# Optimization experiments

Measured on AMD Instinct MI355X. Metric: run time of the kernel, lower is better.

Reference implementation:

```python
import jax, jax.numpy as jnp
import numpy as np

B, S, D, H, E, K = 8, 8192, 256, 1024, 8, 2


def setup_inputs() -> dict:
    key = jax.random.key(0)
    ks = jax.random.split(key, 7)
    s_in = 1.0 / np.sqrt(D)
    s_hid = 1.0 / np.sqrt(H)
    return {
        "x": jax.random.normal(ks[0], (B, S, D), dtype=jnp.float32),
        "Wg": jax.random.uniform(ks[1], (E, D), jnp.float32, -s_in, s_in),
        "bg": jax.random.uniform(ks[2], (E,), jnp.float32, -s_in, s_in),
        "W1": jax.random.uniform(ks[3], (E, H, D), jnp.float32, -s_in, s_in),
        "b1": jax.random.uniform(ks[4], (E, H), jnp.float32, -s_in, s_in),
        "W2": jax.random.uniform(ks[5], (E, D, H), jnp.float32, -s_hid, s_hid),
        "b2": jax.random.uniform(ks[6], (E, D), jnp.float32, -s_hid, s_hid),
    }


def reference(x, Wg, bg, W1, b1, W2, b2):
    # gate: [B,S,E]
    gate_scores = jnp.einsum("bsd,ed->bse", x, Wg) + bg
    topk_scores, topk_idx = jax.lax.top_k(gate_scores, K)  # [B,S,K]
    topk_probs = jax.nn.softmax(topk_scores, axis=-1)      # [B,S,K]
    # combine weight per expert: sum over top-k slots of prob * one_hot(idx)
    combine = jnp.sum(topk_probs[..., None] * jax.nn.one_hot(topk_idx, E, dtype=x.dtype), axis=-2)  # [B,S,E]
    out = jnp.zeros_like(x)
    for e in range(E):  # small fixed loop over experts
        h = jax.nn.relu(jnp.einsum("bsd,hd->bsh", x, W1[e]) + b1[e])
        y = jnp.einsum("bsh,dh->bsd", h, W2[e]) + b2[e]
        out = out + combine[..., e:e + 1] * y
    return out
```

## Files before the change

### kernel.cpp

```cpp
#include <hip/hip_runtime.h>
#include <hip/hip_bf16.h>

#define T_TOKENS 65536
#define D_DIM 256
#define H_DIM 1024
#define E_NUM 8
#define MT 256
#define NTILE (T_TOKENS / MT)
#define HC 32
#define NCHUNK 32
#define GTB 64

typedef __attribute__((ext_vector_type(4))) float f32x4;
typedef __attribute__((ext_vector_type(8))) short s16x8;
typedef __attribute__((ext_vector_type(4))) unsigned int u32x4;
typedef __attribute__((ext_vector_type(4))) unsigned short u16x4;
typedef __attribute__((address_space(3))) unsigned int lds_u32;
typedef const __attribute__((address_space(1))) unsigned int glb_u32;

#define MFMA __builtin_amdgcn_mfma_f32_16x16x32_bf16

__device__ __forceinline__ unsigned short f2bf(float f){
  union { float f; unsigned u; } v; v.f = f;
  unsigned r = v.u + 0x7FFFu + ((v.u >> 16) & 1u);
  return (unsigned short)(r >> 16);
}
__device__ __forceinline__ float bf2f(unsigned short h){
  return __uint_as_float((unsigned)h << 16);
}
__device__ __forceinline__ unsigned cvtpk(float lo, float hi){
  unsigned r;
  asm("v_cvt_pk_bf16_f32 %0, %1, %2" : "=v"(r) : "v"(lo), "v"(hi));
  return r;
}
__device__ __forceinline__ unsigned long long pack4(f32x4 v){
  return (unsigned long long)f2bf(v.x)
       | ((unsigned long long)f2bf(v.y) << 16)
       | ((unsigned long long)f2bf(v.z) << 32)
       | ((unsigned long long)f2bf(v.w) << 48);
}

__device__ __forceinline__ void cvt_unit(int i, const float* __restrict__ W1,
                                         const float* __restrict__ W2,
                                         char* __restrict__ wsw){
  const int N1 = (E_NUM * H_DIM * D_DIM) / 4;
  unsigned long long pk;
  size_t off;
  if (i < N1){
    pk = pack4(((const f32x4*)W1)[i]);
    int idx = i << 2;
    int e  = idx >> 18;
    int h  = (idx >> 8) & (H_DIM - 1);
    int d0 = idx & (D_DIM - 1);
    int c = h >> 5, mi = (h >> 4) & 1, mrow = h & 15;
    int ks = d0 >> 5, qj = (d0 >> 3) & 3, e2 = d0 & 7;
    off = ((size_t)(e * NCHUNK + c) << 15)
        + (size_t)(((ks*2 + mi) << 10) + ((qj*16 + mrow) << 4) + (e2 << 1));
  } else {
    pk = pack4(((const f32x4*)W2)[i - N1]);
    int idx = (i - N1) << 2;
    int e   = idx >> 18;
    int d   = (idx >> 10) & (D_DIM - 1);
    int h0  = idx & (H_DIM - 1);
    int c   = h0 >> 5;
    int h32 = h0 & 31;
    int mi = (h32 >> 4) & 1, qj = (h32 >> 2) & 3;
    off = ((size_t)(e * NCHUNK + c) << 15) + 16384
        + (size_t)(((d >> 4) << 10) + ((qj * 16 + (d & 15)) << 4) + (mi << 3));
  }
  *(unsigned long long*)(wsw + off) = pk;
}

__global__ __launch_bounds__(256) void gate_kernel(
    const float* __restrict__ x, const float* __restrict__ Wg,
    const float* __restrict__ bg,
    const float* __restrict__ W1, const float* __restrict__ W2,
    char* __restrict__ wsw,
    int* __restrict__ counts, int* __restrict__ tok_ids, float* __restrict__ rrec)
{
  __shared__ int lcnt[E_NUM];
  __shared__ int lbase[E_NUM];
  __shared__ unsigned char aexp[GTB * 2];
  __shared__ short         apos[GTB * 2];

  int tid = threadIdx.x, wave = tid >> 6, lane = tid & 63;

  int gthr = blockIdx.x * 256 + tid;
#pragma unroll
  for (int j = 0; j < 4; ++j)
    cvt_unit(gthr + j * ((T_TOKENS / GTB) * 256), W1, W2, wsw);

  if (tid < E_NUM) lcnt[tid] = 0;
  __syncthreads();

  int t0 = blockIdx.x * GTB;
#pragma unroll 1
  for (int i = 0; i < GTB / 4; ++i){
    int tl = wave * (GTB / 4) + i;
    int t = t0 + tl;
    f32x4 xv = *(const f32x4*)(x + (size_t)t * D_DIM + 4*lane);
    float s[E_NUM];
#pragma unroll
    for (int e = 0; e < E_NUM; ++e){
      f32x4 w = *(const f32x4*)(Wg + e*D_DIM + 4*lane);
      s[e] = xv.x*w.x + xv.y*w.y + xv.z*w.z + xv.w*w.w;
    }
#pragma unroll
    for (int off = 32; off; off >>= 1){
#pragma unroll
      for (int e = 0; e < E_NUM; ++e) s[e] += __shfl_xor(s[e], off);
    }
#pragma unroll
    for (int e = 0; e < E_NUM; ++e) s[e] += bg[e];
    int e0 = 0; float v0 = s[0];
#pragma unroll
    for (int e = 1; e < E_NUM; ++e) if (s[e] > v0){ v0 = s[e]; e0 = e; }
    int e1 = -1; float v1 = -3.4e38f;
#pragma unroll
    for (int e = 0; e < E_NUM; ++e){
      if (e == e0) continue;
      if (s[e] > v1){ v1 = s[e]; e1 = e; }
    }
    float ex = __expf(v1 - v0);
    float inv = 1.f / (1.f + ex);
    float p0 = inv, p1 = ex * inv;
    if (lane == 0){
      int li = tl * 2;
      int pos0 = atomicAdd(&lcnt[e0], 1);
      int pos1 = atomicAdd(&lcnt[e1], 1);
      aexp[li]   = (unsigned char)e0; apos[li]   = (short)pos0;
      aexp[li+1] = (unsigned char)e1; apos[li+1] = (short)pos1;
      f32x4 rr; rr.x = p0; rr.y = p1; rr.z = (float)e0; rr.w = (float)e1;
      *(f32x4*)(rrec + (size_t)t * 4) = rr;
    }
  }
  __syncthreads();
  if (tid < E_NUM) lbase[tid] = atomicAdd(counts + tid*16, lcnt[tid]);
  __syncthreads();
  if (tid < GTB * 2){
    int t = t0 + (tid >> 1);
    int e = aexp[tid];
    int idx = lbase[e] + apos[tid];
    tok_ids[e*T_TOKENS + idx] = t | ((tid & 1) << 16);
  }
}

__global__ __launch_bounds__(512, 2) void ffn_kernel(
  const float* __restrict__ x, const char* __restrict__ wsw,
  const float* __restrict__ b1,
  const int* __restrict__ counts, const int* __restrict__ tok_ids,
  unsigned short* __restrict__ yslot)
{
  const int e    = blockIdx.x & 7;
  const int tile = blockIdx.x >> 3;
  const int cnt  = counts[e * 16];
  const int base = tile * MT;
  if (base >= cnt) return;

  __shared__ __align__(1024) unsigned short Ws[2][16384];
  __shared__ __align__(16)   float b1s[H_DIM];
  __shared__ int sTok[MT];

  const int tid = threadIdx.x, wave = tid >> 6, lane = tid & 63;
  const int mrow = lane & 15, qj = lane >> 4;
  const char* wexp = wsw + ((size_t)(e * NCHUNK) << 15);

  auto stage = [&](int c, int buf){
    const char* src = wexp + ((size_t)c << 15);
    char* dst = (char*)&Ws[buf][0];
#pragma unroll
    for (int i = 0; i < 4; ++i){
      int ub = i * 8192 + wave * 1024;
      __builtin_amdgcn_global_load_lds(
        (glb_u32*)(src + ub + lane * 16),
        (lds_u32*)(dst + ub), 16, 0, 0);
    }
  };

  if (tid < MT){
    int idx = base + tid;
    sTok[tid] = (idx < cnt) ? tok_ids[e*T_TOKENS + idx] : -1;
  }
  if (tid < 256) *(f32x4*)&b1s[tid * 4] = ((const f32x4*)(b1 + e*H_DIM))[tid];
  __syncthreads();

  stage(0, 0);

  s16x8 afr[2][8];
#pragma unroll
  for (int ti = 0; ti < 2; ++ti){
    int ent = sTok[wave*32 + ti*16 + mrow];
    int tk = ent & 0xFFFF;
    const f32x4* src = (const f32x4*)(x + (size_t)(ent < 0 ? 0 : tk) * D_DIM);
#pragma unroll
    for (int k = 0; k < 8; ++k){
      f32x4 a = src[k*8 + qj*2];
      f32x4 b = src[k*8 + qj*2 + 1];
      s16x8 f;
      f[0]=(short)f2bf(a.x); f[1]=(short)f2bf(a.y); f[2]=(short)f2bf(a.z); f[3]=(short)f2bf(a.w);
      f[4]=(short)f2bf(b.x); f[5]=(short)f2bf(b.y); f[6]=(short)f2bf(b.z); f[7]=(short)f2bf(b.w);
      if (ent < 0) f = (s16x8)(short)0;
      afr[ti][k] = f;
    }
  }

  const int lb = lane * 16;

  asm volatile("s_waitcnt vmcnt(0) lgkmcnt(0)" ::: "memory");
  __builtin_amdgcn_s_barrier();

  f32x4 yacc[16][2];
#pragma unroll
  for (int m = 0; m < 16; ++m){
    yacc[m][0] = (f32x4){0.f,0.f,0.f,0.f};
    yacc[m][1] = (f32x4){0.f,0.f,0.f,0.f};
  }

  int buf = 0;
#pragma unroll 1
  for (int c = 0; c < NCHUNK; ++c){
    if (c + 1 < NCHUNK) stage(c + 1, buf ^ 1);

    const char* Wb = (const char*)&Ws[buf][0];

    __builtin_amdgcn_s_setprio(1);
    f32x4 hacc[2][2];
    hacc[0][0] = (f32x4){0.f,0.f,0.f,0.f}; hacc[0][1] = (f32x4){0.f,0.f,0.f,0.f};
    hacc[1][0] = (f32x4){0.f,0.f,0.f,0.f}; hacc[1][1] = (f32x4){0.f,0.f,0.f,0.f};
#pragma unroll
    for (int ks = 0; ks < 8; ++ks){
      s16x8 wa = *(const s16x8*)(Wb + lb + (ks*2    )*1024);
      s16x8 wb = *(const s16x8*)(Wb + lb + (ks*2 + 1)*1024);
      hacc[0][0] = MFMA(wa, afr[0][ks], hacc[0][0], 0, 0, 0);
      hacc[0][1] = MFMA(wa, afr[1][ks], hacc[0][1], 0, 0, 0);
      hacc[1][0] = MFMA(wb, afr[0][ks], hacc[1][0], 0, 0, 0);
      hacc[1][1] = MFMA(wb, afr[1][ks], hacc[1][1], 0, 0, 0);
    }
    __builtin_amdgcn_s_setprio(0);

    f32x4 bv0 = *(const f32x4*)&b1s[c*32 + qj*4];
    f32x4 bv1 = *(const f32x4*)&b1s[c*32 + 16 + qj*4];
    s16x8 pb0, pb1;
    {
      f32x4 h0 = hacc[0][0], h1 = hacc[1][0];
      h0.x = fmaxf(h0.x + bv0.x, 0.f); h0.y = fmaxf(h0.y + bv0.y, 0.f);
      h0.z = fmaxf(h0.z + bv0.z, 0.f); h0.w = fmaxf(h0.w + bv0.w, 0.f);
      h1.x = fmaxf(h1.x + bv1.x, 0.f); h1.y = fmaxf(h1.y + bv1.y, 0.f);
      h1.z = fmaxf(h1.z + bv1.z, 0.f); h1.w = fmaxf(h1.w + bv1.w, 0.f);
      u32x4 pw;
      pw.x = cvtpk(h0.x, h0.y); pw.y = cvtpk(h0.z, h0.w);
      pw.z = cvtpk(h1.x, h1.y); pw.w = cvtpk(h1.z, h1.w);
      pb0 = __builtin_bit_cast(s16x8, pw);
    }
    {
      f32x4 h0 = hacc[0][1], h1 = hacc[1][1];
      h0.x = fmaxf(h0.x + bv0.x, 0.f); h0.y = fmaxf(h0.y + bv0.y, 0.f);
      h0.z = fmaxf(h0.z + bv0.z, 0.f); h0.w = fmaxf(h0.w + bv0.w, 0.f);
      h1.x = fmaxf(h1.x + bv1.x, 0.f); h1.y = fmaxf(h1.y + bv1.y, 0.f);
      h1.z = fmaxf(h1.z + bv1.z, 0.f); h1.w = fmaxf(h1.w + bv1.w, 0.f);
      u32x4 pw;
      pw.x = cvtpk(h0.x, h0.y); pw.y = cvtpk(h0.z, h0.w);
      pw.z = cvtpk(h1.x, h1.y); pw.w = cvtpk(h1.z, h1.w);
      pb1 = __builtin_bit_cast(s16x8, pw);
    }

    __builtin_amdgcn_s_setprio(1);
    const char* Wl = Wb + 16384;
#pragma unroll
    for (int m = 0; m < 16; ++m){
      s16x8 lf = *(const s16x8*)(Wl + lb + m*1024);
      yacc[m][0] = MFMA(lf, pb0, yacc[m][0], 0, 0, 0);
      yacc[m][1] = MFMA(lf, pb1, yacc[m][1], 0, 0, 0);
    }
    __builtin_amdgcn_s_setprio(0);

    asm volatile("s_waitcnt vmcnt(0) lgkmcnt(0)" ::: "memory");
    __builtin_amdgcn_s_barrier();
    buf ^= 1;
  }

#pragma unroll
  for (int ti = 0; ti < 2; ++ti){
    int ent = sTok[wave*32 + ti*16 + mrow];
    if (ent < 0) continue;
    int slot = ((ent & 0xFFFF) << 1) | ((ent >> 16) & 1);
    unsigned short* dst = yslot + (size_t)slot * 256;
#pragma unroll
    for (int m = 0; m < 16; ++m){
      unsigned lo = cvtpk(yacc[m][ti][0], yacc[m][ti][1]);
      unsigned hi = cvtpk(yacc[m][ti][2], yacc[m][ti][3]);
      *(unsigned*)(dst + m*16 + qj*4)     = lo;
      *(unsigned*)(dst + m*16 + qj*4 + 2) = hi;
    }
  }
}

__global__ __launch_bounds__(256) void combine_kernel(
    const float* __restrict__ rrec, const float* __restrict__ b2,
    float* __restrict__ out)
{
  int t = blockIdx.x * 4 + (threadIdx.x >> 6);
  int lane = threadIdx.x & 63;
  f32x4 rr = *(const f32x4*)(rrec + (size_t)t * 4);
  float p0 = rr.x, p1 = rr.y;
  int e0 = (int)rr.z, e1 = (int)rr.w;
  const u16x4* s0 = (const u16x4*)((const unsigned short*)out + (size_t)t * 512);
  u16x4 a = s0[lane];
  u16x4 b = s0[64 + lane];
  f32x4 z0 = *(const f32x4*)(b2 + e0*D_DIM + 4*lane);
  f32x4 z1 = *(const f32x4*)(b2 + e1*D_DIM + 4*lane);
  f32x4 o;
  o.x = p0*(bf2f(a.x) + z0.x) + p1*(bf2f(b.x) + z1.x);
  o.y = p0*(bf2f(a.y) + z0.y) + p1*(bf2f(b.y) + z1.y);
  o.z = p0*(bf2f(a.z) + z0.z) + p1*(bf2f(b.z) + z1.z);
  o.w = p0*(bf2f(a.w) + z0.w) + p1*(bf2f(b.w) + z1.w);
  *(f32x4*)(out + (size_t)t * D_DIM + 4*lane) = o;
}

extern "C" void kernel_launch(void* const* d_in, const int* in_sizes, int n_in,
                              void* d_out, int out_size, void* d_ws, size_t ws_size,
                              hipStream_t stream) {
  const float* x  = (const float*)d_in[0];
  const float* Wg = (const float*)d_in[1];
  const float* bg = (const float*)d_in[2];
  const float* W1 = (const float*)d_in[3];
  const float* b1 = (const float*)d_in[4];
  const float* W2 = (const float*)d_in[5];
  const float* b2 = (const float*)d_in[6];
  float* out = (float*)d_out;
  char* ws = (char*)d_ws;

  char*  wsw     = ws;
  int*   counts  = (int*)  (ws + 8388608);
  int*   tok_ids = (int*)  (ws + 8389632);
  float* rrec    = (float*)(ws + 10486784);

  hipMemsetAsync(counts, 0, 512, stream);
  gate_kernel<<<T_TOKENS/GTB, 256, 0, stream>>>(x, Wg, bg, W1, W2, wsw,
                                                counts, tok_ids, rrec);
  ffn_kernel<<<E_NUM * NTILE, 512, 0, stream>>>(x, wsw, b1, counts, tok_ids,
                                                (unsigned short*)d_out);
  combine_kernel<<<T_TOKENS/4, 256, 0, stream>>>(rrec, b2, out);
}
```

Baseline: 296.4 us.

## Halve FFN tile to 128 tokens and pipeline weights through four half-chunk LDS buffers

Shrinks the per-block token tile from 256 to 128 and blocks from 512 to 256 threads. Weight staging is split into half-chunks (W1 part and W2 part) across a 4-deep LDS ring, prefetched three stages ahead with vmcnt-based waits, so each phase only waits for its own half. The goal is finer-grained overlap of weight loads with MFMA work, less LDS per block and more blocks per CU. In exchange each block reuses every weight chunk over half as many tokens, which doubles total weight traffic, and the hand-counted vmcnt waits are fragile.

```diff
diff --git a/kernel.cpp b/kernel.cpp
--- a/kernel.cpp
+++ b/kernel.cpp
@@ -5,7 +5,7 @@
 #define D_DIM 256
 #define H_DIM 1024
 #define E_NUM 8
-#define MT 256
+#define MT 128
 #define NTILE (T_TOKENS / MT)
 #define HC 32
 #define NCHUNK 32
@@ -145,7 +145,7 @@
   }
 }
 
-__global__ __launch_bounds__(512, 2) void ffn_kernel(
+__global__ __launch_bounds__(256, 2) void ffn_kernel(
   const float* __restrict__ x, const char* __restrict__ wsw,
   const float* __restrict__ b1,
   const int* __restrict__ counts, const int* __restrict__ tok_ids,
@@ -157,7 +157,7 @@
   const int base = tile * MT;
   if (base >= cnt) return;
 
-  __shared__ __align__(1024) unsigned short Ws[2][16384];
+  __shared__ __align__(1024) unsigned short Wr[4][8192];
   __shared__ __align__(16)   float b1s[H_DIM];
   __shared__ int sTok[MT];
 
@@ -165,12 +165,12 @@
   const int mrow = lane & 15, qj = lane >> 4;
   const char* wexp = wsw + ((size_t)(e * NCHUNK) << 15);
 
-  auto stage = [&](int c, int buf){
-    const char* src = wexp + ((size_t)c << 15);
-    char* dst = (char*)&Ws[buf][0];
+  auto stage = [&](int j){
+    const char* src = wexp + ((size_t)(j >> 1) << 15) + ((size_t)(j & 1) << 14);
+    char* dst = (char*)&Wr[j & 3][0];
 #pragma unroll
     for (int i = 0; i < 4; ++i){
-      int ub = i * 8192 + wave * 1024;
+      int ub = i * 4096 + wave * 1024;
       __builtin_amdgcn_global_load_lds(
         (glb_u32*)(src + ub + lane * 16),
         (lds_u32*)(dst + ub), 16, 0, 0);
@@ -181,10 +181,8 @@
     int idx = base + tid;
     sTok[tid] = (idx < cnt) ? tok_ids[e*T_TOKENS + idx] : -1;
   }
-  if (tid < 256) *(f32x4*)&b1s[tid * 4] = ((const f32x4*)(b1 + e*H_DIM))[tid];
+  *(f32x4*)&b1s[tid * 4] = ((const f32x4*)(b1 + e*H_DIM))[tid];
   __syncthreads();
-
-  stage(0, 0);
 
   s16x8 afr[2][8];
 #pragma unroll
@@ -203,11 +201,11 @@
       afr[ti][k] = f;
     }
   }
+  asm volatile("s_waitcnt vmcnt(0)" ::: "memory");
+
+  stage(0); stage(1); stage(2);
 
   const int lb = lane * 16;
-
-  asm volatile("s_waitcnt vmcnt(0) lgkmcnt(0)" ::: "memory");
-  __builtin_amdgcn_s_barrier();
 
   f32x4 yacc[16][2];
 #pragma unroll
@@ -215,29 +213,28 @@
     yacc[m][0] = (f32x4){0.f,0.f,0.f,0.f};
     yacc[m][1] = (f32x4){0.f,0.f,0.f,0.f};
   }
-
-  int buf = 0;
-#pragma unroll 1
-  for (int c = 0; c < NCHUNK; ++c){
-    if (c + 1 < NCHUNK) stage(c + 1, buf ^ 1);
-
-    const char* Wb = (const char*)&Ws[buf][0];
-
+  f32x4 hacc[2][2];
+
+  auto phase1 = [&](int c){
+    const char* Wb = (const char*)&Wr[(c & 1) * 2][0];
     __builtin_amdgcn_s_setprio(1);
-    f32x4 hacc[2][2];
-    hacc[0][0] = (f32x4){0.f,0.f,0.f,0.f}; hacc[0][1] = (f32x4){0.f,0.f,0.f,0.f};
-    hacc[1][0] = (f32x4){0.f,0.f,0.f,0.f}; hacc[1][1] = (f32x4){0.f,0.f,0.f,0.f};
+    f32x4 h00 = (f32x4){0.f,0.f,0.f,0.f}, h01 = (f32x4){0.f,0.f,0.f,0.f};
+    f32x4 h10 = (f32x4){0.f,0.f,0.f,0.f}, h11 = (f32x4){0.f,0.f,0.f,0.f};
 #pragma unroll
     for (int ks = 0; ks < 8; ++ks){
       s16x8 wa = *(const s16x8*)(Wb + lb + (ks*2    )*1024);
       s16x8 wb = *(const s16x8*)(Wb + lb + (ks*2 + 1)*1024);
-      hacc[0][0] = MFMA(wa, afr[0][ks], hacc[0][0], 0, 0, 0);
-      hacc[0][1] = MFMA(wa, afr[1][ks], hacc[0][1], 0, 0, 0);
-      hacc[1][0] = MFMA(wb, afr[0][ks], hacc[1][0], 0, 0, 0);
-      hacc[1][1] = MFMA(wb, afr[1][ks], hacc[1][1], 0, 0, 0);
-    }
+      h00 = MFMA(wa, afr[0][ks], h00, 0, 0, 0);
+      h01 = MFMA(wa, afr[1][ks], h01, 0, 0, 0);
+      h10 = MFMA(wb, afr[0][ks], h10, 0, 0, 0);
+      h11 = MFMA(wb, afr[1][ks], h11, 0, 0, 0);
+    }
+    hacc[0][0] = h00; hacc[0][1] = h01;
+    hacc[1][0] = h10; hacc[1][1] = h11;
     __builtin_amdgcn_s_setprio(0);
-
+  };
+
+  auto phase2 = [&](int c){
     f32x4 bv0 = *(const f32x4*)&b1s[c*32 + qj*4];
     f32x4 bv1 = *(const f32x4*)&b1s[c*32 + 16 + qj*4];
     s16x8 pb0, pb1;
@@ -263,9 +260,8 @@
       pw.z = cvtpk(h1.x, h1.y); pw.w = cvtpk(h1.z, h1.w);
       pb1 = __builtin_bit_cast(s16x8, pw);
     }
-
+    const char* Wl = (const char*)&Wr[(c & 1) * 2 + 1][0];
     __builtin_amdgcn_s_setprio(1);
-    const char* Wl = Wb + 16384;
 #pragma unroll
     for (int m = 0; m < 16; ++m){
       s16x8 lf = *(const s16x8*)(Wl + lb + m*1024);
@@ -273,11 +269,30 @@
       yacc[m][1] = MFMA(lf, pb1, yacc[m][1], 0, 0, 0);
     }
     __builtin_amdgcn_s_setprio(0);
-
-    asm volatile("s_waitcnt vmcnt(0) lgkmcnt(0)" ::: "memory");
-    __builtin_amdgcn_s_barrier();
-    buf ^= 1;
-  }
+  };
+
+#define VM_BAR(N) asm volatile("s_waitcnt vmcnt(" #N ")\ns_barrier" ::: "memory")
+#define RD_BAR()  asm volatile("s_waitcnt lgkmcnt(0)\ns_barrier" ::: "memory")
+
+#pragma unroll 1
+  for (int c = 0; c < 30; ++c){
+    stage(2*c + 3);
+    VM_BAR(12);
+    phase1(c);
+    RD_BAR();
+    stage(2*c + 4);
+    VM_BAR(12);
+    phase2(c);
+    RD_BAR();
+  }
+  stage(63);
+  VM_BAR(12);  phase1(30);  RD_BAR();
+  VM_BAR(8);   phase2(30);  RD_BAR();
+  VM_BAR(4);   phase1(31);  RD_BAR();
+  VM_BAR(0);   phase2(31);
+
+#undef VM_BAR
+#undef RD_BAR
 
 #pragma unroll
   for (int ti = 0; ti < 2; ++ti){
@@ -338,7 +353,7 @@
   hipMemsetAsync(counts, 0, 512, stream);
   gate_kernel<<<T_TOKENS/GTB, 256, 0, stream>>>(x, Wg, bg, W1, W2, wsw,
                                                 counts, tok_ids, rrec);
-  ffn_kernel<<<E_NUM * NTILE, 512, 0, stream>>>(x, wsw, b1, counts, tok_ids,
+  ffn_kernel<<<E_NUM * NTILE, 256, 0, stream>>>(x, wsw, b1, counts, tok_ids,
                                                 (unsigned short*)d_out);
   combine_kernel<<<T_TOKENS/4, 256, 0, stream>>>(rrec, b2, out);
 }
```

After: 264.6 us. -10.7%, faster.
